# Kernel tuning notes

Measured on AMD Instinct MI355X. Metric: run time of the kernel, lower is better.

The kernel has to match this reference:

```python
import jax, jax.numpy as jnp
import numpy as np
import math

B, T, L, C = 4, 8, 512, 768
H = 8
HD = C // H  # 96
EPS = 1e-12  # F.normalize eps


def _l2norm(x):
    # F.normalize(x, dim=-1): x / max(||x||2, eps)
    n = jnp.sqrt(jnp.sum(x * x, axis=-1, keepdims=True))
    return x / jnp.maximum(n, EPS)


def setup_inputs() -> dict:
    key = jax.random.key(0)
    ks = jax.random.split(key, 7)
    s = 1.0 / math.sqrt(C)
    x = jax.random.normal(ks[0], (B, T, L, C), dtype=jnp.float32)
    Wq = jax.random.uniform(ks[1], (C, C), jnp.float32, -s, s)
    bq = jax.random.uniform(ks[2], (C,), jnp.float32, -s, s)
    Wkv = jax.random.uniform(ks[3], (C, 2 * C), jnp.float32, -s, s)
    bkv = jax.random.uniform(ks[4], (2 * C,), jnp.float32, -s, s)
    Wm = jax.random.uniform(ks[5], (C, C), jnp.float32, -s, s)
    bm = jax.random.uniform(ks[6], (C,), jnp.float32, -s, s)
    return {"x": x, "Wq": Wq, "bq": bq, "Wkv": Wkv, "bkv": bkv, "Wm": Wm, "bm": bm}


def reference(x, Wq, bq, Wkv, bkv, Wm, bm):
    b, t, l, c = x.shape
    # q: (b,t,l,c) -> (b,t,H,l,hd), L2-normalized over hd
    q = (x @ Wq + bq).reshape(b, t, l, H, HD).transpose(0, 1, 3, 2, 4)
    q = _l2norm(q)
    # kv: (b,t,l,2c) -> (b,t,2H,l,hd); chunk on head axis -> k = heads [0,H), v = heads [H,2H)
    kv = (x @ Wkv + bkv).reshape(b, t, l, 2 * H, HD).transpose(0, 1, 3, 2, 4)
    k = _l2norm(kv[:, :, :H])
    v = _l2norm(kv[:, :, H:])
    # attention (dropout on scores is identity in eval mode)
    scores = jnp.einsum("bthqd,bthkd->bthqk", q, k) / math.sqrt(HD)
    attn = jax.nn.softmax(scores, axis=-1)
    out = jnp.einsum("bthqk,bthkd->bthqd", attn, v)
    # (b,t,H,l,hd) -> (b,t,l,c), output projection (drop2 identity in eval)
    out = out.transpose(0, 1, 3, 2, 4).reshape(b, t, l, c)
    return out @ Wm + bm
```

## Files before the change

kernel.cpp:

```cpp
#include <hip/hip_runtime.h>
#include <hip/hip_bf16.h>


typedef __attribute__((ext_vector_type(8))) short bf16x8;
typedef __attribute__((ext_vector_type(4))) float f32x4;
typedef __attribute__((ext_vector_type(4))) int int4v;

__device__ __forceinline__ float b2f(unsigned short u) {
    return __uint_as_float(((unsigned)u) << 16);
}
__device__ __forceinline__ unsigned short f2b(float f) {
    unsigned u = __float_as_uint(f);
    u = (u + 0x7fffu + ((u >> 16) & 1u)) >> 16;
    return (unsigned short)u;
}

__device__ __forceinline__ void gll16(const unsigned short* g, unsigned short* l) {
    __builtin_amdgcn_global_load_lds((const __attribute__((address_space(1))) unsigned int*)g,
                                     (__attribute__((address_space(3))) unsigned int*)l, 16, 0, 0);
}

#define VMCNT(n) asm volatile("s_waitcnt vmcnt(" #n ")" ::: "memory")
#define BAR()    __builtin_amdgcn_s_barrier()
#define SCHED0() __builtin_amdgcn_sched_barrier(0)
#define PRIO(x)  __builtin_amdgcn_s_setprio(x)

__global__ __launch_bounds__(256) void cast_bf16_k(const float* __restrict__ x,
                                                   unsigned short* __restrict__ xb, int n4) {
    int i = blockIdx.x * 256 + threadIdx.x;
    if (i >= n4) return;
    float4 v = ((const float4*)x)[i];
    ushort4 o;
    o.x = f2b(v.x); o.y = f2b(v.y); o.z = f2b(v.z); o.w = f2b(v.w);
    ((ushort4*)xb)[i] = o;
}

__global__ __launch_bounds__(256) void pack_w_k(const float* __restrict__ Wq,
                                                const float* __restrict__ Wkv,
                                                const float* __restrict__ Wm,
                                                unsigned short* __restrict__ Wt) {
    __shared__ float tile[64][65];
    const int tid = threadIdx.x;
    const int tn = blockIdx.x % 48;
    const int tk = blockIdx.x / 48;
    const int n0 = tn * 64, k0 = tk * 64;
    const float* src; int ldn, coff;
    if (n0 < 768)       { src = Wq;  ldn = 768;  coff = n0; }
    else if (n0 < 2304) { src = Wkv; ldn = 1536; coff = n0 - 768; }
    else                { src = Wm;  ldn = 768;  coff = n0 - 2304; }
    const int j = tid & 63;
    for (int i = tid >> 6; i < 64; i += 4)
        tile[i][j] = src[(k0 + i) * ldn + coff + j];
    __syncthreads();
    const int ii = tid & 63;
    for (int jj = tid >> 6; jj < 64; jj += 4)
        Wt[(long)(n0 + jj) * 768 + k0 + ii] = f2b(tile[ii][jj]);
}

template <int EPI>
__global__ __launch_bounds__(512, 4) void gemm_k(const unsigned short* __restrict__ A,
                                                 const unsigned short* __restrict__ Bt,
                                                 const float* __restrict__ bias0,
                                                 const float* __restrict__ bias1,
                                                 unsigned short* __restrict__ Cb,
                                                 float* __restrict__ Cf,
                                                 int N, int K, int nbn) {
    extern __shared__ unsigned short lds[];
    const int tid = threadIdx.x;
    const int lane = tid & 63, wid = tid >> 6;
    const int wm = wid >> 1, wn = wid & 1;
    const int l15 = lane & 15, g = lane >> 4;

    const int nwg = gridDim.x;
    const int wg = (blockIdx.x & 7) * (nwg >> 3) + (blockIdx.x >> 3);
    const int bm = wg / nbn, bn = wg % nbn;

    const unsigned short* gA = A  + (long)bm * 256 * K;
    const unsigned short* gB = Bt + (long)bn * 128 * K;

    const long sgoff = (long)(tid >> 2) * K + (long)(((tid & 3) ^ ((tid >> 3) & 3)) * 8);
    const int swoff = wid * 512;

#define STAGE_ALL(T, BUFO) do { \
        const long kb0 = (long)(T) * 32; \
        gll16(gB + sgoff + kb0, lds + (BUFO) + 8192 + swoff); \
        gll16(gA + sgoff + kb0, lds + (BUFO) + swoff); \
        gll16(gA + sgoff + kb0 + (long)128 * K, lds + (BUFO) + 4096 + swoff); \
    } while (0)

    const int slot8 = (g ^ ((l15 >> 1) & 3)) * 8;
    f32x4 acc[4][4] = {};
    const int nkt = K >> 5;

    STAGE_ALL(0, 0);

    int cur = 0, nxt = 12288;
    for (int t = 0; t < nkt; ++t) {
        if (t + 1 < nkt) STAGE_ALL(t + 1, nxt);
        if (t < nkt - 1) { VMCNT(3); } else { VMCNT(0); }
        BAR(); SCHED0();

        bf16x8 af[4], bv[4];
#pragma unroll
        for (int mf = 0; mf < 4; mf++)
            af[mf] = *(const bf16x8*)&lds[cur + (wm * 64 + mf * 16 + l15) * 32 + slot8];
#pragma unroll
        for (int nf = 0; nf < 4; nf++)
            bv[nf] = *(const bf16x8*)&lds[cur + 8192 + (wn * 64 + nf * 16 + l15) * 32 + slot8];
        PRIO(1);
#pragma unroll
        for (int mf = 0; mf < 4; mf++)
#pragma unroll
            for (int nf = 0; nf < 4; nf++)
                acc[mf][nf] = __builtin_amdgcn_mfma_f32_16x16x32_bf16(af[mf], bv[nf], acc[mf][nf], 0, 0, 0);
        PRIO(0);
        BAR();
        const int tmp = cur; cur = nxt; nxt = tmp;
    }
#undef STAGE_ALL

    float bvv[4];
#pragma unroll
    for (int nf = 0; nf < 4; nf++) {
        const int col = bn * 128 + wn * 64 + nf * 16 + l15;
        bvv[nf] = (EPI == 0) ? ((col < 768) ? bias0[col] : bias1[col - 768]) : bias0[col];
    }
#pragma unroll
    for (int mf = 0; mf < 4; mf++) {
#pragma unroll
        for (int r = 0; r < 4; r++) {
            const long row = bm * 256 + wm * 64 + mf * 16 + g * 4 + r;
#pragma unroll
            for (int nf = 0; nf < 4; nf++) {
                const float v = acc[mf][nf][r] + bvv[nf];
                if (EPI == 0) {
                    const unsigned hh = f2b(v);
                    const unsigned oo = __shfl_xor((int)hh, 1);
                    if (!(lane & 1))
                        *(unsigned*)&Cb[row * N + bn * 128 + wn * 64 + nf * 16 + l15] =
                            (hh & 0xffffu) | (oo << 16);
                } else {
                    Cf[row * N + bn * 128 + wn * 64 + nf * 16 + l15] = v;
                }
            }
        }
    }
}

__global__ __launch_bounds__(512, 6) void gemm128_k(const unsigned short* __restrict__ A,
                                                    const unsigned short* __restrict__ Bt,
                                                    const float* __restrict__ bias0,
                                                    float* __restrict__ Cf,
                                                    int N, int K, int nbn) {
    extern __shared__ unsigned short lds[];
    const int tid = threadIdx.x;
    const int lane = tid & 63, wid = tid >> 6;
    const int wm = wid >> 2, wn = wid & 3;
    const int l15 = lane & 15, g = lane >> 4;

    const int nwg = gridDim.x;
    const int wg = (blockIdx.x & 7) * (nwg >> 3) + (blockIdx.x >> 3);
    const int bm = wg / nbn, bn = wg % nbn;

    const unsigned short* gA = A  + (long)bm * 128 * K;
    const unsigned short* gB = Bt + (long)bn * 128 * K;

    const long sgoff = (long)(tid >> 2) * K + (long)(((tid & 3) ^ ((tid >> 3) & 3)) * 8);
    const int swoff = wid * 512;

#define STAGE2(T, BUFO) do { \
        const long kb0 = (long)(T) * 32; \
        gll16(gB + sgoff + kb0, lds + (BUFO) + 4096 + swoff); \
        gll16(gA + sgoff + kb0, lds + (BUFO) + swoff); \
    } while (0)

    const int slot8 = (g ^ ((l15 >> 1) & 3)) * 8;
    f32x4 acc[4][2] = {};
    const int nkt = K >> 5;

    STAGE2(0, 0);
    STAGE2(1, 8192);

    int cur = 0, nx1 = 8192, nx2 = 16384;
    for (int t = 0; t < nkt; ++t) {
        if (t < nkt - 1) { VMCNT(2); } else { VMCNT(0); }
        BAR(); SCHED0();
        if (t + 2 < nkt) STAGE2(t + 2, nx2);

        bf16x8 af[4], bv[2];
#pragma unroll
        for (int mf = 0; mf < 4; mf++)
            af[mf] = *(const bf16x8*)&lds[cur + (wm * 64 + mf * 16 + l15) * 32 + slot8];
#pragma unroll
        for (int nf = 0; nf < 2; nf++)
            bv[nf] = *(const bf16x8*)&lds[cur + 4096 + (wn * 32 + nf * 16 + l15) * 32 + slot8];
        PRIO(1);
#pragma unroll
        for (int mf = 0; mf < 4; mf++)
#pragma unroll
            for (int nf = 0; nf < 2; nf++)
                acc[mf][nf] = __builtin_amdgcn_mfma_f32_16x16x32_bf16(af[mf], bv[nf], acc[mf][nf], 0, 0, 0);
        PRIO(0);
        const int tmp = cur; cur = nx1; nx1 = nx2; nx2 = tmp;
    }
#undef STAGE2

    float bvv[2];
#pragma unroll
    for (int nf = 0; nf < 2; nf++)
        bvv[nf] = bias0[bn * 128 + wn * 32 + nf * 16 + l15];
#pragma unroll
    for (int mf = 0; mf < 4; mf++) {
#pragma unroll
        for (int r = 0; r < 4; r++) {
            const long row = bm * 128 + wm * 64 + mf * 16 + g * 4 + r;
#pragma unroll
            for (int nf = 0; nf < 2; nf++)
                Cf[row * N + bn * 128 + wn * 32 + nf * 16 + l15] = acc[mf][nf][r] + bvv[nf];
        }
    }
}

__global__ __launch_bounds__(256) void knvn_k(const unsigned short* __restrict__ qkv,
                                              float* __restrict__ kinv,
                                              float* __restrict__ vinv) {
    const int tid = threadIdx.x, lane = tid & 63, w = tid >> 6;
    const int s = blockIdx.x * 4 + w;
    const int row = s >> 3, h = s & 7;
    const unsigned short* pk = qkv + (long)row * 2304 + 768 + h * 96;
    float k0 = 0.f, k1 = 0.f, v0 = 0.f, v1 = 0.f;
    if (lane < 48) {
        unsigned a = *(const unsigned*)(pk + lane * 2);
        unsigned b = *(const unsigned*)(pk + 768 + lane * 2);
        k0 = b2f((unsigned short)(a & 0xffffu)); k1 = b2f((unsigned short)(a >> 16));
        v0 = b2f((unsigned short)(b & 0xffffu)); v1 = b2f((unsigned short)(b >> 16));
    }
    float sk = k0 * k0 + k1 * k1;
    float sv = v0 * v0 + v1 * v1;
#pragma unroll
    for (int m = 1; m < 64; m <<= 1) { sk += __shfl_xor(sk, m); sv += __shfl_xor(sv, m); }
    if (lane == 0) {
        kinv[h * 16384 + row] = 1.f / fmaxf(sqrtf(sk), 1e-12f);
        vinv[h * 16384 + row] = 1.f / fmaxf(sqrtf(sv), 1e-12f);
    }
}

__global__ __launch_bounds__(512, 2) void attn_k(const unsigned short* __restrict__ qkv,
                                                 const float* __restrict__ kinv,
                                                 const float* __restrict__ vinv,
                                                 unsigned short* __restrict__ obuf) {
    constexpr float SCALE = 0.1020620726159658f;
    __shared__ unsigned short Qs[128 * 104];
    __shared__ unsigned short Ks[64 * 104];
    __shared__ unsigned short Vt[96 * 72];
    __shared__ float kinv_s[2][64], vinv_s[2][64];

    const int tid = threadIdx.x, lane = tid & 63, w = tid >> 6;
    const int bid0 = blockIdx.x;
    const int bid = (bid0 & 7) * 128 + (bid0 >> 3);
    const int qt = bid & 3, h = (bid >> 2) & 7, bt = bid >> 5;
    const long rowbase = (long)bt * 512 * 2304 + h * 96;
    const int l15 = lane & 15;
    const int g = lane >> 4;
    const int ko = g * 8;

    for (int j = 0; j < 3; j++) {
        const int c = tid + j * 512;
        const int r = c / 12, d8 = (c % 12) * 8;
        *(int4v*)&Qs[r * 104 + d8] = *(const int4v*)&qkv[rowbase + (long)(qt * 128 + r) * 2304 + d8];
    }
    if (tid < 256) {
#pragma unroll
        for (int j = 0; j < 3; j++) {
            const int c = tid + j * 256;
            const int r = c / 12, d8 = (c % 12) * 8;
            *(int4v*)&Ks[r * 104 + d8] = *(const int4v*)&qkv[rowbase + 768 + (long)r * 2304 + d8];
        }
    } else {
        const int tid2 = tid - 256;
#pragma unroll
        for (int j = 0; j < 2; j++) {
            const int c = tid2 + j * 256;
            if (c < 384) {
                const int kp = c & 31, d8c = c >> 5;
                const unsigned short* vsrc = &qkv[rowbase + 1536 + (long)(2 * kp) * 2304 + d8c * 8];
                int4v v0 = *(const int4v*)vsrc;
                int4v v1 = *(const int4v*)(vsrc + 2304);
                const unsigned short* p0 = (const unsigned short*)&v0;
                const unsigned short* p1 = (const unsigned short*)&v1;
#pragma unroll
                for (int i = 0; i < 8; i++)
                    *(unsigned*)&Vt[(d8c * 8 + i) * 72 + 2 * kp] =
                        (unsigned)p0[i] | ((unsigned)p1[i] << 16);
            }
        }
    }
    if (tid < 64)       kinv_s[0][tid]      = kinv[h * 16384 + bt * 512 + tid];
    else if (tid < 128) vinv_s[0][tid - 64] = vinv[h * 16384 + bt * 512 + tid - 64];
    __syncthreads();

    bf16x8 qf[3];
#pragma unroll
    for (int ks = 0; ks < 3; ks++)
        qf[ks] = *(const bf16x8*)&Qs[(w * 16 + l15) * 104 + ks * 32 + ko];
    float ssq = 0.f;
#pragma unroll
    for (int ks = 0; ks < 3; ks++)
#pragma unroll
        for (int j = 0; j < 8; j++) {
            const float f = b2f((unsigned short)qf[ks][j]);
            ssq += f * f;
        }
    ssq += __shfl_xor(ssq, 16);
    ssq += __shfl_xor(ssq, 32);
    const float qs = SCALE / fmaxf(sqrtf(ssq), 1e-12f);

    float l_run = 0.f;
    f32x4 oacc[6] = {};

    for (int kt = 0; kt < 8; kt++) {
        const int cb = kt & 1, nb = cb ^ 1;

        int4v preg[4];
        float tn = 0.f;
        if (kt < 7) {
            if (tid < 256) {
                const long kb = rowbase + 768 + (long)((kt + 1) * 64) * 2304;
#pragma unroll
                for (int j = 0; j < 3; j++) {
                    const int c = tid + j * 256;
                    preg[j] = *(const int4v*)&qkv[kb + (long)(c / 12) * 2304 + (c % 12) * 8];
                }
            } else {
                const int tid2 = tid - 256;
                const long vb = rowbase + 1536 + (long)((kt + 1) * 64) * 2304;
#pragma unroll
                for (int j = 0; j < 2; j++) {
                    const int c = tid2 + j * 256;
                    if (c < 384) {
                        const int kp = c & 31, d8c = c >> 5;
                        const unsigned short* vsrc = &qkv[vb + (long)(2 * kp) * 2304 + d8c * 8];
                        preg[2 * j]     = *(const int4v*)vsrc;
                        preg[2 * j + 1] = *(const int4v*)(vsrc + 2304);
                    }
                }
            }
            if (tid < 64)       tn = kinv[h * 16384 + bt * 512 + (kt + 1) * 64 + tid];
            else if (tid < 128) tn = vinv[h * 16384 + bt * 512 + (kt + 1) * 64 + tid - 64];
        }

        f32x4 sacc[4] = {};
#pragma unroll
        for (int ks = 0; ks < 3; ks++) {
#pragma unroll
            for (int kf = 0; kf < 4; kf++) {
                bf16x8 af = *(const bf16x8*)&Ks[(kf * 16 + l15) * 104 + ks * 32 + ko];
                sacc[kf] = __builtin_amdgcn_mfma_f32_16x16x32_bf16(af, qf[ks], sacc[kf], 0, 0, 0);
            }
        }

        float p[16];
        float s = 0.f;
#pragma unroll
        for (int kf = 0; kf < 4; kf++)
#pragma unroll
            for (int r = 0; r < 4; r++) {
                const float pv = __expf(sacc[kf][r] * qs * kinv_s[cb][kf * 16 + g * 4 + r]);
                s += pv;
                p[kf * 4 + r] = pv * vinv_s[cb][kf * 16 + g * 4 + r];
            }
        s += __shfl_xor(s, 16);
        s += __shfl_xor(s, 32);
        l_run += s;

        {
            unsigned* prow = (unsigned*)&Qs[(w * 16 + l15) * 104];
#pragma unroll
            for (int kf = 0; kf < 4; kf++)
#pragma unroll
                for (int rp = 0; rp < 2; rp++) {
                    unsigned pk = (unsigned)f2b(p[kf * 4 + 2 * rp]) |
                                  ((unsigned)f2b(p[kf * 4 + 2 * rp + 1]) << 16);
                    prow[kf * 8 + g * 2 + rp] = pk;
                }
        }

#pragma unroll
        for (int ks = 0; ks < 2; ks++) {
            bf16x8 pa = *(const bf16x8*)&Qs[(w * 16 + l15) * 104 + ks * 32 + ko];
#pragma unroll
            for (int nf = 0; nf < 6; nf++) {
                bf16x8 vb = *(const bf16x8*)&Vt[(nf * 16 + l15) * 72 + ks * 32 + ko];
                oacc[nf] = __builtin_amdgcn_mfma_f32_16x16x32_bf16(pa, vb, oacc[nf], 0, 0, 0);
            }
        }
        __syncthreads();

        if (kt < 7) {
            if (tid < 256) {
#pragma unroll
                for (int j = 0; j < 3; j++) {
                    const int c = tid + j * 256;
                    *(int4v*)&Ks[(c / 12) * 104 + (c % 12) * 8] = preg[j];
                }
            } else {
                const int tid2 = tid - 256;
#pragma unroll
                for (int j = 0; j < 2; j++) {
                    const int c = tid2 + j * 256;
                    if (c < 384) {
                        const int kp = c & 31, d8c = c >> 5;
                        const unsigned short* p0 = (const unsigned short*)&preg[2 * j];
                        const unsigned short* p1 = (const unsigned short*)&preg[2 * j + 1];
#pragma unroll
                        for (int i = 0; i < 8; i++)
                            *(unsigned*)&Vt[(d8c * 8 + i) * 72 + 2 * kp] =
                                (unsigned)p0[i] | ((unsigned)p1[i] << 16);
                    }
                }
            }
            if (tid < 64)       kinv_s[nb][tid]      = tn;
            else if (tid < 128) vinv_s[nb][tid - 64] = tn;
            __syncthreads();
        }
    }

    const float inv = 1.f / l_run;
    float invr[4];
#pragma unroll
    for (int r = 0; r < 4; r++) invr[r] = __shfl(inv, g * 4 + r);
#pragma unroll
    for (int r = 0; r < 4; r++) {
        const int row = w * 16 + g * 4 + r;
        const long gr = ((long)(bt * 512 + qt * 128 + row)) * 768 + h * 96;
#pragma unroll
        for (int nf = 0; nf < 6; nf++)
            obuf[gr + nf * 16 + l15] = f2b(oacc[nf][r] * invr[r]);
    }
}

extern "C" void kernel_launch(void* const* d_in, const int* in_sizes, int n_in,
                              void* d_out, int out_size, void* d_ws, size_t ws_size,
                              hipStream_t stream) {
    const float* x   = (const float*)d_in[0];
    const float* Wq  = (const float*)d_in[1];
    const float* bq  = (const float*)d_in[2];
    const float* Wkv = (const float*)d_in[3];
    const float* bkv = (const float*)d_in[4];
    const float* Wm  = (const float*)d_in[5];
    const float* bm  = (const float*)d_in[6];
    float* out = (float*)d_out;

    char* ws = (char*)d_ws;
    unsigned short* xb  = (unsigned short*)ws;
    float*          vinv = (float*)ws;
    float*          kinv = (float*)(ws + 524288);
    unsigned short* wt  = (unsigned short*)(ws + 25165824);
    unsigned short* qkv = (unsigned short*)(ws + 29884416);
    unsigned short* ob  = (unsigned short*)(ws + 105381888);

    static bool attr_set = false;
    if (!attr_set) {
        hipFuncSetAttribute((const void*)gemm_k<0>, hipFuncAttributeMaxDynamicSharedMemorySize, 49152);
        hipFuncSetAttribute((const void*)gemm128_k, hipFuncAttributeMaxDynamicSharedMemorySize, 49152);
        attr_set = true;
    }

    cast_bf16_k<<<dim3(12288), dim3(256), 0, stream>>>(x, xb, 3145728);
    pack_w_k<<<dim3(576), dim3(256), 0, stream>>>(Wq, Wkv, Wm, wt);
    gemm_k<0><<<dim3(1152), dim3(512), 49152, stream>>>(xb, wt, bq, bkv, qkv, nullptr, 2304, 768, 18);
    knvn_k<<<dim3(32768), dim3(256), 0, stream>>>(qkv, kinv, vinv);
    attn_k<<<dim3(1024), dim3(512), 0, stream>>>(qkv, kinv, vinv, ob);
    gemm128_k<<<dim3(768), dim3(512), 49152, stream>>>(ob, wt + (long)2304 * 768, bm, out, 768, 768, 6);
}
```

Before: 198.0 us.

## Triple-buffer QKV GEMM with 64-wide K tiles and split interleaved prefetch

Rewrites the QKV projection GEMM to use 64-element K tiles with a three-stage LDS ring buffer (147 KB dynamic shared memory). Each iteration issues the next-next tile's global-to-LDS loads in two halves interleaved between the two MFMA phases. The goal is to hide global memory latency better and halve the number of barriers per K. The cost is much larger LDS use, which limits occupancy to about one or two workgroups per CU. It also uses a wider 8-chunk XOR swizzle.

```diff
diff --git a/kernel.cpp b/kernel.cpp
--- a/kernel.cpp
+++ b/kernel.cpp
@@ -57,14 +57,12 @@
         Wt[(long)(n0 + jj) * 768 + k0 + ii] = f2b(tile[ii][jj]);
 }
 
-template <int EPI>
-__global__ __launch_bounds__(512, 4) void gemm_k(const unsigned short* __restrict__ A,
-                                                 const unsigned short* __restrict__ Bt,
-                                                 const float* __restrict__ bias0,
-                                                 const float* __restrict__ bias1,
-                                                 unsigned short* __restrict__ Cb,
-                                                 float* __restrict__ Cf,
-                                                 int N, int K, int nbn) {
+__global__ __launch_bounds__(512, 2) void gemm8_k(const unsigned short* __restrict__ A,
+                                                  const unsigned short* __restrict__ Bt,
+                                                  const float* __restrict__ bias0,
+                                                  const float* __restrict__ bias1,
+                                                  unsigned short* __restrict__ Cb,
+                                                  int N, int K, int nbn) {
     extern __shared__ unsigned short lds[];
     const int tid = threadIdx.x;
     const int lane = tid & 63, wid = tid >> 6;
@@ -78,52 +76,85 @@
     const unsigned short* gA = A  + (long)bm * 256 * K;
     const unsigned short* gB = Bt + (long)bn * 128 * K;
 
-    const long sgoff = (long)(tid >> 2) * K + (long)(((tid & 3) ^ ((tid >> 3) & 3)) * 8);
-    const int swoff = wid * 512;
-
-#define STAGE_ALL(T, BUFO) do { \
-        const long kb0 = (long)(T) * 32; \
-        gll16(gB + sgoff + kb0, lds + (BUFO) + 8192 + swoff); \
-        gll16(gA + sgoff + kb0, lds + (BUFO) + swoff); \
-        gll16(gA + sgoff + kb0 + (long)128 * K, lds + (BUFO) + 4096 + swoff); \
-    } while (0)
-
-    const int slot8 = (g ^ ((l15 >> 1) & 3)) * 8;
+    const long srowK = (long)(tid >> 3) * K;
+    const int schunk = ((tid & 7) ^ ((tid >> 3) & 7)) * 8;
+    const int w512 = wid * 512;
+
+#define STA(T, BO, a) gll16(gA + (long)(T) * 64 + (long)((a) * 64) * K + srowK + schunk, \
+                            lds + (BO) + (a) * 4096 + w512)
+#define STB(T, BO, b2) gll16(gB + (long)(T) * 64 + (long)((b2) * 64) * K + srowK + schunk, \
+                             lds + (BO) + 16384 + (b2) * 4096 + w512)
+
+    const int slot0 = ((0 * 4 + g) ^ (l15 & 7)) * 8;
+    const int slot1 = ((1 * 4 + g) ^ (l15 & 7)) * 8;
+    const int arow = wm * 4096 + l15 * 64;
+    const int brow = 16384 + wn * 4096 + l15 * 64;
+
     f32x4 acc[4][4] = {};
-    const int nkt = K >> 5;
-
-    STAGE_ALL(0, 0);
-
-    int cur = 0, nxt = 12288;
+    const int nkt = K >> 6;
+
+    STA(0, 0, 0); STA(0, 0, 1); STA(0, 0, 2); STA(0, 0, 3); STB(0, 0, 0); STB(0, 0, 1);
+    STA(1, 24576, 0); STA(1, 24576, 1); STA(1, 24576, 2); STA(1, 24576, 3);
+    STB(1, 24576, 0); STB(1, 24576, 1);
+
     for (int t = 0; t < nkt; ++t) {
-        if (t + 1 < nkt) STAGE_ALL(t + 1, nxt);
-        if (t < nkt - 1) { VMCNT(3); } else { VMCNT(0); }
+        const int cur = (t % 3) * 24576;
+        const int stg = ((t + 2) % 3) * 24576;
+        const bool pf = (t + 2 < nkt);
+
+        if (t < nkt - 1) { VMCNT(6); } else { VMCNT(0); }
         BAR(); SCHED0();
 
-        bf16x8 af[4], bv[4];
+        bf16x8 af[4][2], bf[2][2];
+#pragma unroll
+        for (int mf = 0; mf < 4; mf++) {
+            af[mf][0] = *(const bf16x8*)&lds[cur + arow + mf * 1024 + slot0];
+            af[mf][1] = *(const bf16x8*)&lds[cur + arow + mf * 1024 + slot1];
+        }
+#pragma unroll
+        for (int nf = 0; nf < 2; nf++) {
+            bf[nf][0] = *(const bf16x8*)&lds[cur + brow + nf * 1024 + slot0];
+            bf[nf][1] = *(const bf16x8*)&lds[cur + brow + nf * 1024 + slot1];
+        }
+        if (pf) { STA(t + 2, stg, 0); STA(t + 2, stg, 1); STA(t + 2, stg, 2); }
+        SCHED0();
+        PRIO(1);
 #pragma unroll
         for (int mf = 0; mf < 4; mf++)
-            af[mf] = *(const bf16x8*)&lds[cur + (wm * 64 + mf * 16 + l15) * 32 + slot8];
-#pragma unroll
-        for (int nf = 0; nf < 4; nf++)
-            bv[nf] = *(const bf16x8*)&lds[cur + 8192 + (wn * 64 + nf * 16 + l15) * 32 + slot8];
-        PRIO(1);
-#pragma unroll
-        for (int mf = 0; mf < 4; mf++)
-#pragma unroll
-            for (int nf = 0; nf < 4; nf++)
-                acc[mf][nf] = __builtin_amdgcn_mfma_f32_16x16x32_bf16(af[mf], bv[nf], acc[mf][nf], 0, 0, 0);
+#pragma unroll
+            for (int nf = 0; nf < 2; nf++)
+#pragma unroll
+                for (int kk = 0; kk < 2; kk++)
+                    acc[mf][nf] = __builtin_amdgcn_mfma_f32_16x16x32_bf16(
+                        af[mf][kk], bf[nf][kk], acc[mf][nf], 0, 0, 0);
         PRIO(0);
         BAR();
-        const int tmp = cur; cur = nxt; nxt = tmp;
-    }
-#undef STAGE_ALL
+#pragma unroll
+        for (int nf = 0; nf < 2; nf++) {
+            bf[nf][0] = *(const bf16x8*)&lds[cur + brow + (nf + 2) * 1024 + slot0];
+            bf[nf][1] = *(const bf16x8*)&lds[cur + brow + (nf + 2) * 1024 + slot1];
+        }
+        if (pf) { STA(t + 2, stg, 3); STB(t + 2, stg, 0); STB(t + 2, stg, 1); }
+        SCHED0();
+        PRIO(1);
+#pragma unroll
+        for (int mf = 0; mf < 4; mf++)
+#pragma unroll
+            for (int nf = 0; nf < 2; nf++)
+#pragma unroll
+                for (int kk = 0; kk < 2; kk++)
+                    acc[mf][nf + 2] = __builtin_amdgcn_mfma_f32_16x16x32_bf16(
+                        af[mf][kk], bf[nf][kk], acc[mf][nf + 2], 0, 0, 0);
+        PRIO(0);
+    }
+#undef STA
+#undef STB
 
     float bvv[4];
 #pragma unroll
     for (int nf = 0; nf < 4; nf++) {
         const int col = bn * 128 + wn * 64 + nf * 16 + l15;
-        bvv[nf] = (EPI == 0) ? ((col < 768) ? bias0[col] : bias1[col - 768]) : bias0[col];
+        bvv[nf] = (col < 768) ? bias0[col] : bias1[col - 768];
     }
 #pragma unroll
     for (int mf = 0; mf < 4; mf++) {
@@ -133,15 +164,11 @@
 #pragma unroll
             for (int nf = 0; nf < 4; nf++) {
                 const float v = acc[mf][nf][r] + bvv[nf];
-                if (EPI == 0) {
-                    const unsigned hh = f2b(v);
-                    const unsigned oo = __shfl_xor((int)hh, 1);
-                    if (!(lane & 1))
-                        *(unsigned*)&Cb[row * N + bn * 128 + wn * 64 + nf * 16 + l15] =
-                            (hh & 0xffffu) | (oo << 16);
-                } else {
-                    Cf[row * N + bn * 128 + wn * 64 + nf * 16 + l15] = v;
-                }
+                const unsigned hh = f2b(v);
+                const unsigned oo = __shfl_xor((int)hh, 1);
+                if (!(lane & 1))
+                    *(unsigned*)&Cb[row * N + bn * 128 + wn * 64 + nf * 16 + l15] =
+                        (hh & 0xffffu) | (oo << 16);
             }
         }
     }
@@ -461,14 +488,14 @@
 
     static bool attr_set = false;
     if (!attr_set) {
-        hipFuncSetAttribute((const void*)gemm_k<0>, hipFuncAttributeMaxDynamicSharedMemorySize, 49152);
+        hipFuncSetAttribute((const void*)gemm8_k, hipFuncAttributeMaxDynamicSharedMemorySize, 147456);
         hipFuncSetAttribute((const void*)gemm128_k, hipFuncAttributeMaxDynamicSharedMemorySize, 49152);
         attr_set = true;
     }
 
     cast_bf16_k<<<dim3(12288), dim3(256), 0, stream>>>(x, xb, 3145728);
     pack_w_k<<<dim3(576), dim3(256), 0, stream>>>(Wq, Wkv, Wm, wt);
-    gemm_k<0><<<dim3(1152), dim3(512), 49152, stream>>>(xb, wt, bq, bkv, qkv, nullptr, 2304, 768, 18);
+    gemm8_k<<<dim3(1152), dim3(512), 147456, stream>>>(xb, wt, bq, bkv, qkv, 2304, 768, 18);
     knvn_k<<<dim3(32768), dim3(256), 0, stream>>>(qkv, kinv, vinv);
     attn_k<<<dim3(1024), dim3(512), 0, stream>>>(qkv, kinv, vinv, ob);
     gemm128_k<<<dim3(768), dim3(512), 49152, stream>>>(ob, wt + (long)2304 * 768, bm, out, 768, 768, 6);
```

After: 211.9 us. 7.1% more time.
